# Performance work log

Hardware: AMD Instinct MI355X
Metric: run time of the kernel (lower is better)

The kernel has to match this reference:

```python
import jax, jax.numpy as jnp
import numpy as np

NUM_HEADS = 16
KEY_SIZE = 64
D_MODEL = 1024


def setup_inputs() -> dict:
    key = jax.random.key(0)
    ks = jax.random.split(key, 9)
    B, S = 2, 2048
    HK = NUM_HEADS * KEY_SIZE
    s = 1.0 / np.sqrt(D_MODEL)
    return {
        "x": jax.random.normal(ks[0], (B, S, D_MODEL), dtype=jnp.float32),
        "Wq": jax.random.normal(ks[1], (D_MODEL, HK), dtype=jnp.float32) * s,
        "bq": jax.random.normal(ks[2], (HK,), dtype=jnp.float32) * 0.02,
        "Wk": jax.random.normal(ks[3], (D_MODEL, HK), dtype=jnp.float32) * s,
        "bk": jax.random.normal(ks[4], (HK,), dtype=jnp.float32) * 0.02,
        "Wv": jax.random.normal(ks[5], (D_MODEL, HK), dtype=jnp.float32) * s,
        "bv": jax.random.normal(ks[6], (HK,), dtype=jnp.float32) * 0.02,
        "Wo": jax.random.normal(ks[7], (HK, D_MODEL), dtype=jnp.float32) * s,
        "bo": jax.random.normal(ks[8], (D_MODEL,), dtype=jnp.float32) * 0.02,
    }


def reference(x, Wq, bq, Wk, bk, Wv, bv, Wo, bo):
    B, S, _ = x.shape
    H, K = NUM_HEADS, KEY_SIZE
    # QKV projections -> (B, H, S, K)
    def proj(W, b):
        return (x @ W + b).reshape(B, S, H, K).transpose(0, 2, 1, 3)
    q = proj(Wq, bq)
    k = proj(Wk, bk)
    v = proj(Wv, bv)
    scale = jnp.sqrt(jnp.float32(K))
    scores = jnp.einsum('bhsk,bhtk->bhst', q, k) / scale  # (B,H,S,S)
    attn = jax.nn.softmax(scores, axis=-1)
    out = jnp.einsum('bhst,bhtk->bhsk', attn, v)  # (B,H,S,K)
    out = out.transpose(0, 2, 1, 3).reshape(B, S, H * K)
    return out @ Wo + bo
```

## Files before the change

kernel.cpp:

```cpp
#include <hip/hip_runtime.h>


#define NH 16
#define KS 64
#define DM 1024
#define BB 2
#define SS 2048
#define NT (BB*SS)
#define HKD 1024
#define L2E 1.44269504088896340736f

typedef __attribute__((ext_vector_type(4))) float floatx4;
typedef __attribute__((ext_vector_type(8))) short short8;

__device__ __forceinline__ unsigned short f2b(float f) {
  unsigned u = __builtin_bit_cast(unsigned, f);
  u = (u + 0x7fffu + ((u >> 16) & 1u)) >> 16;
  return (unsigned short)u;
}

__device__ __forceinline__ floatx4 mfma16(short8 a, short8 b, floatx4 c) {
  return __builtin_amdgcn_mfma_f32_16x16x32_bf16(a, b, c, 0, 0, 0);
}

__device__ __forceinline__ void async16(const void* g, void* l) {
  __builtin_amdgcn_global_load_lds(
      (const __attribute__((address_space(1))) unsigned int*)g,
      (__attribute__((address_space(3))) unsigned int*)l, 16, 0, 0);
}

__global__ void cast_x_kernel(const float* __restrict__ x, unsigned short* __restrict__ xb) {
  int i = (blockIdx.x * 256 + threadIdx.x) * 4;
  float4 v = *(const float4*)(x + i);
  ushort4 o;
  o.x = f2b(v.x); o.y = f2b(v.y); o.z = f2b(v.z); o.w = f2b(v.w);
  *(ushort4*)(xb + i) = o;
}

__global__ void transw_kernel(const float* __restrict__ Wq, const float* __restrict__ Wk,
                              const float* __restrict__ Wv, const float* __restrict__ Wo,
                              unsigned short* __restrict__ wqt, unsigned short* __restrict__ wkt,
                              unsigned short* __restrict__ wvt, unsigned short* __restrict__ wot) {
  const float* W; unsigned short* Wt;
  if (blockIdx.z == 0)      { W = Wq; Wt = wqt; }
  else if (blockIdx.z == 1) { W = Wk; Wt = wkt; }
  else if (blockIdx.z == 2) { W = Wv; Wt = wvt; }
  else                      { W = Wo; Wt = wot; }
  __shared__ __align__(16) unsigned short tile[64][80];
  int k0 = blockIdx.x * 64, n0 = blockIdx.y * 64;
  int t = threadIdx.x;
  int c0 = (t & 15) * 4, r = t >> 4;
  #pragma unroll
  for (int p = 0; p < 4; ++p) {
    int rr = r + p * 16;
    float4 v = *(const float4*)(W + (k0 + rr) * DM + n0 + c0);
    tile[c0 + 0][rr] = f2b(v.x);
    tile[c0 + 1][rr] = f2b(v.y);
    tile[c0 + 2][rr] = f2b(v.z);
    tile[c0 + 3][rr] = f2b(v.w);
  }
  __syncthreads();
  int cc0 = (t & 7) * 8, rn = t >> 3;
  #pragma unroll
  for (int p = 0; p < 2; ++p) {
    int nn = rn + p * 32;
    *(short8*)(Wt + (n0 + nn) * DM + k0 + cc0) = *(const short8*)(&tile[nn][cc0]);
  }
}

__global__ __launch_bounds__(256) void gemm_qkv_kernel(
    const unsigned short* __restrict__ xb,
    const unsigned short* __restrict__ wqt, const unsigned short* __restrict__ wkt,
    const unsigned short* __restrict__ wvt,
    const float* __restrict__ bq, const float* __restrict__ bk, const float* __restrict__ bv,
    unsigned short* __restrict__ qb, unsigned short* __restrict__ kbuf,
    unsigned short* __restrict__ vbuf) {
  __shared__ __align__(16) unsigned short As[8192], Bs[8192];
  const unsigned short* Bt; const float* bias; unsigned short* dst; float scale;
  if (blockIdx.z == 0)      { Bt = wqt; bias = bq; dst = qb;   scale = 0.125f * L2E; }
  else if (blockIdx.z == 1) { Bt = wkt; bias = bk; dst = kbuf; scale = 1.0f; }
  else                      { Bt = wvt; bias = bv; dst = vbuf; scale = 1.0f; }
  int m0 = blockIdx.x * 128, n0 = blockIdx.y * 128;
  int t = threadIdx.x, w = t >> 6, lane = t & 63, cl = lane & 15, quad = lane >> 4;
  int clm = cl & 7;
  int wr = (w >> 1) * 64, wc = (w & 1) * 64;
  floatx4 acc[4][4];
  #pragma unroll
  for (int i = 0; i < 4; ++i)
    #pragma unroll
    for (int j = 0; j < 4; ++j)
      acc[i][j] = floatx4{0.f, 0.f, 0.f, 0.f};

  for (int kc = 0; kc < DM / 64; ++kc) {
    __syncthreads();
    #pragma unroll
    for (int i = 0; i < 4; ++i) {
      int c = i * 256 + t;
      int row = c >> 3, col8 = (c & 7) ^ (row & 7);
      async16(xb + (m0 + row) * DM + kc * 64 + col8 * 8, &As[c * 8]);
      async16(Bt + (n0 + row) * DM + kc * 64 + col8 * 8, &Bs[c * 8]);
    }
    asm volatile("s_waitcnt vmcnt(0)" ::: "memory");
    __syncthreads();
    #pragma unroll
    for (int kk = 0; kk < 2; ++kk) {
      short8 a[4], b[4];
      #pragma unroll
      for (int i = 0; i < 4; ++i)
        a[i] = *(const short8*)&As[(wr + i * 16 + cl) * 64 + (((kk * 4 + quad) ^ clm) * 8)];
      #pragma unroll
      for (int j = 0; j < 4; ++j)
        b[j] = *(const short8*)&Bs[(wc + j * 16 + cl) * 64 + (((kk * 4 + quad) ^ clm) * 8)];
      #pragma unroll
      for (int i = 0; i < 4; ++i)
        #pragma unroll
        for (int j = 0; j < 4; ++j)
          acc[i][j] = mfma16(a[i], b[j], acc[i][j]);
    }
  }
  int h = (n0 + wc) >> 6;
  #pragma unroll
  for (int j = 0; j < 4; ++j) {
    float bj = bias[n0 + wc + j * 16 + cl];
    int kd = j * 16 + cl;
    #pragma unroll
    for (int i = 0; i < 4; ++i)
      #pragma unroll
      for (int r = 0; r < 4; ++r) {
        int token = m0 + wr + i * 16 + quad * 4 + r;
        int bz = token >> 11, s = token & (SS - 1);
        float val = (acc[i][j][r] + bj) * scale;
        dst[(((bz * NH + h) * SS + s) << 6) + kd] = f2b(val);
      }
  }
}

__global__ void transv_kernel(const unsigned short* __restrict__ v,
                              unsigned short* __restrict__ vt) {
  __shared__ __align__(16) unsigned short tile[64][80];
  int s0 = blockIdx.x * 64, bh = blockIdx.y;
  int t = threadIdx.x;
  int kd0 = (t & 7) * 8, sl = t >> 3;
  #pragma unroll
  for (int p = 0; p < 2; ++p) {
    int sr = sl + p * 32;
    short8 vv = *(const short8*)(v + (bh * SS + s0 + sr) * KS + kd0);
    #pragma unroll
    for (int q = 0; q < 8; ++q) tile[kd0 + q][sr] = ((unsigned short*)&vv)[q];
  }
  __syncthreads();
  int sc0 = (t & 7) * 8, kl = t >> 3;
  #pragma unroll
  for (int p = 0; p < 2; ++p) {
    int kk = kl + p * 32;
    *(short8*)(vt + (bh * KS + kk) * SS + s0 + sc0) = *(const short8*)(&tile[kk][sc0]);
  }
}

__global__ __launch_bounds__(256) void attn_kernel(
    const unsigned short* __restrict__ Q, const unsigned short* __restrict__ Kb,
    const unsigned short* __restrict__ Vt, unsigned short* __restrict__ AO) {
  __shared__ __align__(16) unsigned short Ks[2][4096], Vs[2][4096];
  __shared__ __align__(16) unsigned short Ps[4][2304];
  int t = threadIdx.x, w = t >> 6, lane = t & 63, cl = lane & 15, quad = lane >> 4;
  int clm = cl & 7;
  int h = blockIdx.y, bz = blockIdx.z, bh = bz * NH + h;
  int q0 = blockIdx.x * 128 + w * 32;
  const unsigned short* Qp = Q + (bh * SS + q0) * KS;
  const unsigned short* Kp = Kb + bh * SS * KS;
  const unsigned short* Vp = Vt + bh * KS * SS;
  unsigned short* p_w = Ps[w];

  short8 qa[2][2];
  #pragma unroll
  for (int qt = 0; qt < 2; ++qt)
    #pragma unroll
    for (int c = 0; c < 2; ++c)
      qa[qt][c] = *(const short8*)(Qp + (qt * 16 + cl) * KS + c * 32 + quad * 8);

  float l[2][4];
  floatx4 oa[2][4];
  #pragma unroll
  for (int qt = 0; qt < 2; ++qt) {
    #pragma unroll
    for (int r = 0; r < 4; ++r) l[qt][r] = 0.f;
    #pragma unroll
    for (int j = 0; j < 4; ++j) oa[qt][j] = floatx4{0.f, 0.f, 0.f, 0.f};
  }

  auto stage = [&](int tile, int buf) {
    const unsigned short* kp = Kp + (tile * 64) * KS;
    #pragma unroll
    for (int i = 0; i < 2; ++i) {
      int c = i * 256 + t;
      int row = c >> 3, col8 = (c & 7) ^ (row & 7);
      async16(kp + row * KS + col8 * 8, &Ks[buf][c * 8]);
    }
    #pragma unroll
    for (int i = 0; i < 2; ++i) {
      int c = i * 256 + t;
      int d = c >> 3, col8 = (c & 7) ^ (d & 7);
      async16(Vp + d * SS + tile * 64 + col8 * 8, &Vs[buf][c * 8]);
    }
  };
  stage(0, 0);
  stage(1, 1);

  const int NTILES = SS / 64;
  for (int it = 0; it < NTILES; ++it) {
    int cur = it & 1;
    if (it < NTILES - 1) asm volatile("s_waitcnt vmcnt(4)" ::: "memory");
    else                 asm volatile("s_waitcnt vmcnt(0)" ::: "memory");
    __syncthreads();

    floatx4 s[2][4];
    #pragma unroll
    for (int kt = 0; kt < 4; ++kt) {
      short8 kb0 = *(const short8*)&Ks[cur][(kt * 16 + cl) * 64 + ((quad ^ clm) * 8)];
      short8 kb1 = *(const short8*)&Ks[cur][(kt * 16 + cl) * 64 + (((4 + quad) ^ clm) * 8)];
      #pragma unroll
      for (int qt = 0; qt < 2; ++qt) {
        floatx4 z = {0.f, 0.f, 0.f, 0.f};
        s[qt][kt] = mfma16(qa[qt][1], kb1, mfma16(qa[qt][0], kb0, z));
      }
    }
    #pragma unroll
    for (int qt = 0; qt < 2; ++qt)
      #pragma unroll
      for (int kt = 0; kt < 4; ++kt) {
        int colsw = ((kt ^ quad) << 4) + cl;
        #pragma unroll
        for (int r = 0; r < 4; ++r) {
          float p = __builtin_amdgcn_exp2f(s[qt][kt][r]);
          unsigned u = __builtin_bit_cast(unsigned, p) & 0xffff0000u;
          l[qt][r] += __builtin_bit_cast(float, u);
          p_w[qt * 1152 + (quad * 4 + r) * 72 + colsw] = (unsigned short)(u >> 16);
        }
      }
    asm volatile("s_waitcnt lgkmcnt(0)" ::: "memory");
    short8 pa[2][2];
    #pragma unroll
    for (int qt = 0; qt < 2; ++qt)
      #pragma unroll
      for (int c = 0; c < 2; ++c) {
        int cb = (c * 32 + quad * 8) ^ ((cl >> 2) << 4);
        pa[qt][c] = *(const short8*)(p_w + qt * 1152 + cl * 72 + cb);
      }
    #pragma unroll
    for (int j = 0; j < 4; ++j) {
      short8 vb0 = *(const short8*)&Vs[cur][(j * 16 + cl) * 64 + ((quad ^ clm) * 8)];
      short8 vb1 = *(const short8*)&Vs[cur][(j * 16 + cl) * 64 + (((4 + quad) ^ clm) * 8)];
      #pragma unroll
      for (int qt = 0; qt < 2; ++qt)
        oa[qt][j] = mfma16(pa[qt][1], vb1, mfma16(pa[qt][0], vb0, oa[qt][j]));
    }
    __syncthreads();
    if (it + 2 < NTILES) stage(it + 2, cur);
  }

  #pragma unroll
  for (int qt = 0; qt < 2; ++qt) {
    float inv[4];
    #pragma unroll
    for (int r = 0; r < 4; ++r) {
      float rs = l[qt][r];
      rs += __shfl_xor(rs, 1);
      rs += __shfl_xor(rs, 2);
      rs += __shfl_xor(rs, 4);
      rs += __shfl_xor(rs, 8);
      inv[r] = 1.0f / rs;
    }
    #pragma unroll
    for (int j = 0; j < 4; ++j)
      #pragma unroll
      for (int r = 0; r < 4; ++r) {
        int s = q0 + qt * 16 + quad * 4 + r;
        AO[(bz * SS + s) * DM + h * KS + j * 16 + cl] = f2b(oa[qt][j][r] * inv[r]);
      }
  }
}

__global__ __launch_bounds__(128) void gemm_out_kernel(
    const unsigned short* __restrict__ ao, const unsigned short* __restrict__ wot,
    const float* __restrict__ bo, float* __restrict__ out) {
  __shared__ __align__(16) unsigned short As[8192], Bs[4096];
  int m0 = blockIdx.x * 128, n0 = blockIdx.y * 64;
  int t = threadIdx.x, w = t >> 6, lane = t & 63, cl = lane & 15, quad = lane >> 4;
  int clm = cl & 7;
  int wr = w * 64;
  floatx4 acc[4][4];
  #pragma unroll
  for (int i = 0; i < 4; ++i)
    #pragma unroll
    for (int j = 0; j < 4; ++j)
      acc[i][j] = floatx4{0.f, 0.f, 0.f, 0.f};

  for (int kc = 0; kc < HKD / 64; ++kc) {
    __syncthreads();
    #pragma unroll
    for (int i = 0; i < 8; ++i) {
      int c = i * 128 + t;
      int row = c >> 3, col8 = (c & 7) ^ (row & 7);
      async16(ao + (m0 + row) * HKD + kc * 64 + col8 * 8, &As[c * 8]);
    }
    #pragma unroll
    for (int i = 0; i < 4; ++i) {
      int c = i * 128 + t;
      int row = c >> 3, col8 = (c & 7) ^ (row & 7);
      async16(wot + (n0 + row) * HKD + kc * 64 + col8 * 8, &Bs[c * 8]);
    }
    asm volatile("s_waitcnt vmcnt(0)" ::: "memory");
    __syncthreads();
    #pragma unroll
    for (int kk = 0; kk < 2; ++kk) {
      short8 a[4], b[4];
      #pragma unroll
      for (int i = 0; i < 4; ++i)
        a[i] = *(const short8*)&As[(wr + i * 16 + cl) * 64 + (((kk * 4 + quad) ^ clm) * 8)];
      #pragma unroll
      for (int j = 0; j < 4; ++j)
        b[j] = *(const short8*)&Bs[(j * 16 + cl) * 64 + (((kk * 4 + quad) ^ clm) * 8)];
      #pragma unroll
      for (int i = 0; i < 4; ++i)
        #pragma unroll
        for (int j = 0; j < 4; ++j)
          acc[i][j] = mfma16(a[i], b[j], acc[i][j]);
    }
  }
  #pragma unroll
  for (int j = 0; j < 4; ++j) {
    float bj = bo[n0 + j * 16 + cl];
    #pragma unroll
    for (int i = 0; i < 4; ++i)
      #pragma unroll
      for (int r = 0; r < 4; ++r) {
        int token = m0 + wr + i * 16 + quad * 4 + r;
        out[token * DM + n0 + j * 16 + cl] = acc[i][j][r] + bj;
      }
  }
}

extern "C" void kernel_launch(void* const* d_in, const int* in_sizes, int n_in,
                              void* d_out, int out_size, void* d_ws, size_t ws_size,
                              hipStream_t stream) {
  const float* x  = (const float*)d_in[0];
  const float* Wq = (const float*)d_in[1];
  const float* bq = (const float*)d_in[2];
  const float* Wk = (const float*)d_in[3];
  const float* bk = (const float*)d_in[4];
  const float* Wv = (const float*)d_in[5];
  const float* bv = (const float*)d_in[6];
  const float* Wo = (const float*)d_in[7];
  const float* bo = (const float*)d_in[8];
  float* out = (float*)d_out;
  char* ws = (char*)d_ws;
  unsigned short* xb  = (unsigned short*)(ws);
  unsigned short* wqt = (unsigned short*)(ws + (8ull  << 20));
  unsigned short* wkt = (unsigned short*)(ws + (10ull << 20));
  unsigned short* wvt = (unsigned short*)(ws + (12ull << 20));
  unsigned short* wot = (unsigned short*)(ws + (14ull << 20));
  unsigned short* qb  = (unsigned short*)(ws + (16ull << 20));
  unsigned short* kbf = (unsigned short*)(ws + (24ull << 20));
  unsigned short* vbf = (unsigned short*)(ws + (32ull << 20));
  unsigned short* vt  = (unsigned short*)(ws + (40ull << 20));
  unsigned short* ao  = (unsigned short*)(ws + (48ull << 20));

  hipLaunchKernelGGL(cast_x_kernel, dim3(NT * DM / 1024), dim3(256), 0, stream, x, xb);
  hipLaunchKernelGGL(transw_kernel, dim3(16, 16, 4), dim3(256), 0, stream,
                     Wq, Wk, Wv, Wo, wqt, wkt, wvt, wot);
  hipLaunchKernelGGL(gemm_qkv_kernel, dim3(NT / 128, HKD / 128, 3), dim3(256), 0, stream,
                     xb, wqt, wkt, wvt, bq, bk, bv, qb, kbf, vbf);
  hipLaunchKernelGGL(transv_kernel, dim3(SS / 64, BB * NH), dim3(256), 0, stream, vbf, vt);
  hipLaunchKernelGGL(attn_kernel, dim3(SS / 128, NH, BB), dim3(256), 0, stream, qb, kbf, vt, ao);
  hipLaunchKernelGGL(gemm_out_kernel, dim3(NT / 128, DM / 64), dim3(128), 0, stream, ao, wot, bo, out);
}
```

Measured before the change: 221.9 us.

## Transpose attention MFMA operands and halve query rows per wave

The attention kernel now handles 16 query rows per wave instead of 32, which doubles the grid to 1024 blocks. It also swaps the MFMA operand order so the score and output tiles come out transposed. With that layout each lane owns one query row, so the P tile is written to LDS as packed 8-byte stores and the row sum needs only two shuffles. Output stores are packed as well. The aim is fewer scalar LDS writes and shuffles, plus more blocks for occupancy, but each K/V tile loaded into LDS is now reused by half as many query rows, which doubles K/V traffic.

```diff
diff --git a/kernel.cpp b/kernel.cpp
--- a/kernel.cpp
+++ b/kernel.cpp
@@ -161,32 +161,25 @@
     const unsigned short* __restrict__ Q, const unsigned short* __restrict__ Kb,
     const unsigned short* __restrict__ Vt, unsigned short* __restrict__ AO) {
   __shared__ __align__(16) unsigned short Ks[2][4096], Vs[2][4096];
-  __shared__ __align__(16) unsigned short Ps[4][2304];
+  __shared__ __align__(16) unsigned short Ps[4][1024];
   int t = threadIdx.x, w = t >> 6, lane = t & 63, cl = lane & 15, quad = lane >> 4;
   int clm = cl & 7;
   int h = blockIdx.y, bz = blockIdx.z, bh = bz * NH + h;
-  int q0 = blockIdx.x * 128 + w * 32;
+  int q0 = blockIdx.x * 64 + w * 16;
   const unsigned short* Qp = Q + (bh * SS + q0) * KS;
   const unsigned short* Kp = Kb + bh * SS * KS;
   const unsigned short* Vp = Vt + bh * KS * SS;
   unsigned short* p_w = Ps[w];
 
-  short8 qa[2][2];
-  #pragma unroll
-  for (int qt = 0; qt < 2; ++qt)
-    #pragma unroll
-    for (int c = 0; c < 2; ++c)
-      qa[qt][c] = *(const short8*)(Qp + (qt * 16 + cl) * KS + c * 32 + quad * 8);
-
-  float l[2][4];
-  floatx4 oa[2][4];
-  #pragma unroll
-  for (int qt = 0; qt < 2; ++qt) {
-    #pragma unroll
-    for (int r = 0; r < 4; ++r) l[qt][r] = 0.f;
-    #pragma unroll
-    for (int j = 0; j < 4; ++j) oa[qt][j] = floatx4{0.f, 0.f, 0.f, 0.f};
-  }
+  short8 qa[2];
+  #pragma unroll
+  for (int c = 0; c < 2; ++c)
+    qa[c] = *(const short8*)(Qp + cl * KS + c * 32 + quad * 8);
+
+  float l = 0.f;
+  floatx4 oa[4];
+  #pragma unroll
+  for (int j = 0; j < 4; ++j) oa[j] = floatx4{0.f, 0.f, 0.f, 0.f};
 
   auto stage = [&](int tile, int buf) {
     const unsigned short* kp = Kp + (tile * 64) * KS;
@@ -213,70 +206,56 @@
     else                 asm volatile("s_waitcnt vmcnt(0)" ::: "memory");
     __syncthreads();
 
-    floatx4 s[2][4];
+    floatx4 s[4];
     #pragma unroll
     for (int kt = 0; kt < 4; ++kt) {
       short8 kb0 = *(const short8*)&Ks[cur][(kt * 16 + cl) * 64 + ((quad ^ clm) * 8)];
       short8 kb1 = *(const short8*)&Ks[cur][(kt * 16 + cl) * 64 + (((4 + quad) ^ clm) * 8)];
-      #pragma unroll
-      for (int qt = 0; qt < 2; ++qt) {
-        floatx4 z = {0.f, 0.f, 0.f, 0.f};
-        s[qt][kt] = mfma16(qa[qt][1], kb1, mfma16(qa[qt][0], kb0, z));
+      floatx4 z = {0.f, 0.f, 0.f, 0.f};
+      s[kt] = mfma16(kb1, qa[1], mfma16(kb0, qa[0], z));
+    }
+    #pragma unroll
+    for (int kt = 0; kt < 4; ++kt) {
+      unsigned u[4];
+      #pragma unroll
+      for (int r = 0; r < 4; ++r) {
+        float p = __builtin_amdgcn_exp2f(s[kt][r]);
+        u[r] = __builtin_bit_cast(unsigned, p) & 0xffff0000u;
+        l += __builtin_bit_cast(float, u[r]);
       }
-    }
-    #pragma unroll
-    for (int qt = 0; qt < 2; ++qt)
-      #pragma unroll
-      for (int kt = 0; kt < 4; ++kt) {
-        int colsw = ((kt ^ quad) << 4) + cl;
-        #pragma unroll
-        for (int r = 0; r < 4; ++r) {
-          float p = __builtin_amdgcn_exp2f(s[qt][kt][r]);
-          unsigned u = __builtin_bit_cast(unsigned, p) & 0xffff0000u;
-          l[qt][r] += __builtin_bit_cast(float, u);
-          p_w[qt * 1152 + (quad * 4 + r) * 72 + colsw] = (unsigned short)(u >> 16);
-        }
-      }
+      uint2 pk;
+      pk.x = (u[0] >> 16) | u[1];
+      pk.y = (u[2] >> 16) | u[3];
+      int off = cl * 64 + (((kt * 2 + (quad >> 1)) ^ clm) * 8) + (quad & 1) * 4;
+      *(uint2*)(p_w + off) = pk;
+    }
     asm volatile("s_waitcnt lgkmcnt(0)" ::: "memory");
-    short8 pa[2][2];
-    #pragma unroll
-    for (int qt = 0; qt < 2; ++qt)
-      #pragma unroll
-      for (int c = 0; c < 2; ++c) {
-        int cb = (c * 32 + quad * 8) ^ ((cl >> 2) << 4);
-        pa[qt][c] = *(const short8*)(p_w + qt * 1152 + cl * 72 + cb);
-      }
+    short8 pa[2];
+    #pragma unroll
+    for (int c = 0; c < 2; ++c)
+      pa[c] = *(const short8*)(p_w + cl * 64 + (((c * 4 + quad) ^ clm) * 8));
     #pragma unroll
     for (int j = 0; j < 4; ++j) {
       short8 vb0 = *(const short8*)&Vs[cur][(j * 16 + cl) * 64 + ((quad ^ clm) * 8)];
       short8 vb1 = *(const short8*)&Vs[cur][(j * 16 + cl) * 64 + (((4 + quad) ^ clm) * 8)];
-      #pragma unroll
-      for (int qt = 0; qt < 2; ++qt)
-        oa[qt][j] = mfma16(pa[qt][1], vb1, mfma16(pa[qt][0], vb0, oa[qt][j]));
+      oa[j] = mfma16(vb1, pa[1], mfma16(vb0, pa[0], oa[j]));
     }
     __syncthreads();
     if (it + 2 < NTILES) stage(it + 2, cur);
   }
 
-  #pragma unroll
-  for (int qt = 0; qt < 2; ++qt) {
-    float inv[4];
-    #pragma unroll
-    for (int r = 0; r < 4; ++r) {
-      float rs = l[qt][r];
-      rs += __shfl_xor(rs, 1);
-      rs += __shfl_xor(rs, 2);
-      rs += __shfl_xor(rs, 4);
-      rs += __shfl_xor(rs, 8);
-      inv[r] = 1.0f / rs;
-    }
-    #pragma unroll
-    for (int j = 0; j < 4; ++j)
-      #pragma unroll
-      for (int r = 0; r < 4; ++r) {
-        int s = q0 + qt * 16 + quad * 4 + r;
-        AO[(bz * SS + s) * DM + h * KS + j * 16 + cl] = f2b(oa[qt][j][r] * inv[r]);
-      }
+  l += __shfl_xor(l, 16);
+  l += __shfl_xor(l, 32);
+  float inv = 1.0f / l;
+  unsigned short* aop = AO + (bz * SS + q0 + cl) * DM + h * KS + quad * 4;
+  #pragma unroll
+  for (int j = 0; j < 4; ++j) {
+    unsigned short b0 = f2b(oa[j][0] * inv), b1 = f2b(oa[j][1] * inv);
+    unsigned short b2 = f2b(oa[j][2] * inv), b3 = f2b(oa[j][3] * inv);
+    uint2 pk;
+    pk.x = (unsigned)b0 | ((unsigned)b1 << 16);
+    pk.y = (unsigned)b2 | ((unsigned)b3 << 16);
+    *(uint2*)(aop + j * 16) = pk;
   }
 }
 
@@ -371,6 +350,6 @@
   hipLaunchKernelGGL(gemm_qkv_kernel, dim3(NT / 128, HKD / 128, 3), dim3(256), 0, stream,
                      xb, wqt, wkt, wvt, bq, bk, bv, qb, kbf, vbf);
   hipLaunchKernelGGL(transv_kernel, dim3(SS / 64, BB * NH), dim3(256), 0, stream, vbf, vt);
-  hipLaunchKernelGGL(attn_kernel, dim3(SS / 128, NH, BB), dim3(256), 0, stream, qb, kbf, vt, ao);
+  hipLaunchKernelGGL(attn_kernel, dim3(SS / 64, NH, BB), dim3(256), 0, stream, qb, kbf, vt, ao);
   hipLaunchKernelGGL(gemm_out_kernel, dim3(NT / 128, DM / 64), dim3(128), 0, stream, ao, wot, bo, out);
 }
```

New measurement: 213.5 us. 1.04x faster.
